# Kernel optimization log

Hardware: AMD Instinct MI355X
Metric: run time of the kernel (lower is better)

The kernel has to match this reference:

```python
import jax, jax.numpy as jnp
import numpy as np

EPS = 1e-5
NUM_CLUSTERS = 64


def _bn(x, g, b, m, v):
    # eval-mode BatchNorm over channel (last) axis
    return (x - m) * (g * jax.lax.rsqrt(v + EPS)) + b


def _segment_max(feat, choice, num_clusters):
    # feat: [B, N, C], choice: [B, N] -> [B, K, C] (amax per cluster, -inf if empty)
    def one(f, c):
        init = jnp.full((num_clusters, f.shape[-1]), -jnp.inf, dtype=f.dtype)
        return init.at[c].max(f)
    return jax.vmap(one)(feat, choice)


def setup_inputs() -> dict:
    key = jax.random.key(0)
    ks = jax.random.split(key, 8)
    B, N, K, OUT = 32, 8192, NUM_CLUSTERS, 384
    s = lambda fan: 1.0 / np.sqrt(fan)
    return {
        "xyz": jax.random.normal(ks[0], (B, N, 3), jnp.float32),
        "choice": jax.random.randint(ks[1], (B, N), 0, K, jnp.int32),
        "w1": jax.random.normal(ks[2], (128, 3), jnp.float32) * s(3),
        "b1": jnp.zeros((128,), jnp.float32),
        "bn1_g": jnp.ones((128,), jnp.float32),
        "bn1_b": jnp.zeros((128,), jnp.float32),
        "bn1_m": jnp.zeros((128,), jnp.float32),
        "bn1_v": jnp.ones((128,), jnp.float32),
        "w2": jax.random.normal(ks[3], (256, 128), jnp.float32) * s(128),
        "b2": jnp.zeros((256,), jnp.float32),
        "w3": jax.random.normal(ks[4], (512, 512), jnp.float32) * s(512),
        "b3": jnp.zeros((512,), jnp.float32),
        "bn2_g": jnp.ones((512,), jnp.float32),
        "bn2_b": jnp.zeros((512,), jnp.float32),
        "bn2_m": jnp.zeros((512,), jnp.float32),
        "bn2_v": jnp.ones((512,), jnp.float32),
        "w4": jax.random.normal(ks[5], (OUT, 512), jnp.float32) * s(512),
        "b4": jnp.zeros((OUT,), jnp.float32),
    }


def reference(xyz, choice, w1, b1, bn1_g, bn1_b, bn1_m, bn1_v, w2, b2,
              w3, b3, bn2_g, bn2_b, bn2_m, bn2_v, w4, b4):
    # first_conv: 1x1 conv == per-point linear. xyz: [B,N,3]
    h = jnp.einsum("bnc,oc->bno", xyz, w1) + b1            # [B,N,128]
    h = jax.nn.relu(_bn(h, bn1_g, bn1_b, bn1_m, bn1_v))
    feat = jnp.einsum("bnc,oc->bno", h, w2) + b2            # [B,N,256]
    # cluster amax pooling + gather-broadcast back to points
    fg = _segment_max(feat, choice, NUM_CLUSTERS)           # [B,K,256]
    fg_pts = jnp.take_along_axis(fg, choice[..., None], axis=1)  # [B,N,256]
    f = jnp.concatenate([fg_pts, feat], axis=-1)            # [B,N,512]
    # second_conv
    h2 = jnp.einsum("bnc,oc->bno", f, w3) + b3              # [B,N,512]
    h2 = jax.nn.relu(_bn(h2, bn2_g, bn2_b, bn2_m, bn2_v))
    out = jnp.einsum("bnc,oc->bno", h2, w4) + b4            # [B,N,out_dim]
    return _segment_max(out, choice, NUM_CLUSTERS)          # [B,K,out_dim]
```

## Files before the change

### kernel.cpp

```cpp
#include <hip/hip_runtime.h>
#include <hip/hip_bf16.h>

typedef unsigned short u16;
typedef __attribute__((ext_vector_type(8))) short short8;
typedef __attribute__((ext_vector_type(4))) float f32x4;

#define EPSV 1e-5f
#define ENC_NINF 0x007FFFFFu

__device__ __forceinline__ float bf2f(u16 u) {
    union { unsigned int i; float f; } v; v.i = ((unsigned int)u) << 16; return v.f;
}
__device__ __forceinline__ u16 f2bf(float f) {
    union { float f; unsigned int i; } v; v.f = f;
    unsigned int x = v.i;
    return (u16)((x + 0x7FFFu + ((x >> 16) & 1u)) >> 16);
}
__device__ __forceinline__ unsigned int encbf(u16 u) {
    unsigned int f = ((unsigned int)u) << 16;
    return (f & 0x80000000u) ? ~f : (f | 0x80000000u);
}
__device__ __forceinline__ float dec(unsigned int u) {
    union { float f; unsigned int uu; } v;
    v.uu = (u & 0x80000000u) ? (u & 0x7FFFFFFFu) : ~u;
    return v.f;
}

__device__ __forceinline__ void async16(const u16* g, u16* l) {
    __builtin_amdgcn_global_load_lds((const __attribute__((address_space(1))) void*)g,
                                     (__attribute__((address_space(3))) void*)l,
                                     16, 0, 0);
}

__global__ __launch_bounds__(256) void k_fillf(float* __restrict__ o, int n, float val)
{
    int i = blockIdx.x * 256 + threadIdx.x;
    if (i < n) o[i] = val;
}

struct Ptrs { const void* p[17]; int off[18]; int chN; };

__global__ __launch_bounds__(256) void k_repack(Ptrs P, const void* __restrict__ chSrc,
                                                int* __restrict__ chi, u16* __restrict__ rp,
                                                unsigned int* __restrict__ initp, int nU)
{
    const unsigned int* probe = (const unsigned int*)P.p[9];
    int cnt = 0;
#pragma unroll
    for (int i = 0; i < 64; ++i) {
        unsigned int lo = probe[i] & 0xFFFFu;
        if (((lo >> 7) & 0xFFu) >= 0x80u) ++cnt;
    }
    const bool is_f32 = (cnt > 8);

    const unsigned int* cp = (const unsigned int*)chSrc;
    int z = 0; unsigned int mx = 0;
    for (int i = 0; i < 1024; ++i) {
        unsigned int w = cp[i];
        z += (w == 0u);
        mx = (w > mx) ? w : mx;
    }
    const int chMode = (mx >= 64u) ? 2 : ((z > 300) ? 1 : 0);

    const int stride = gridDim.x * 256;
    const int gid0 = blockIdx.x * 256 + threadIdx.x;

    const int totalF = P.off[17];
    for (int g = gid0; g < totalF; g += stride) {
        int t = 0;
        while (g >= P.off[t + 1]) ++t;
        int off = g - P.off[t];
        u16 v;
        if (is_f32) v = f2bf(((const float*)P.p[t])[off]);
        else        v = ((const u16*)P.p[t])[off];
        rp[g] = v;
    }
    for (int i = gid0; i < P.chN; i += stride) {
        int v;
        if (chMode == 1)      v = (int)((const long long*)chSrc)[i];
        else if (chMode == 2) v = (int)((const float*)chSrc)[i];
        else                  v = ((const int*)chSrc)[i];
        chi[i] = v & 63;
    }
    for (int i = gid0; i < nU; i += stride) initp[i] = ENC_NINF;
}

__global__ __launch_bounds__(256) void k_sort(const int* __restrict__ chi,
                                              int* __restrict__ schoice,
                                              int* __restrict__ perm)
{
    __shared__ int hist[64];
    __shared__ int base[64];
    const int b = blockIdx.x, tid = threadIdx.x;
    if (tid < 64) hist[tid] = 0;
    __syncthreads();
    const int o = b << 13;
    for (int i = tid; i < 8192; i += 256) atomicAdd(&hist[chi[o + i]], 1);
    __syncthreads();
    if (tid == 0) {
        int s = 0;
        for (int k = 0; k < 64; ++k) { base[k] = s; s += hist[k]; }
    }
    __syncthreads();
    for (int i = tid; i < 8192; i += 256) {
        int k = chi[o + i];
        int pos = atomicAdd(&base[k], 1);
        schoice[o + pos] = k;
        perm[o + pos] = o + i;
    }
}

__global__ __launch_bounds__(256, 2) void g1_feat(
    const u16* __restrict__ xyz, const u16* __restrict__ w1, const u16* __restrict__ b1,
    const u16* __restrict__ g1v, const u16* __restrict__ bb1,
    const u16* __restrict__ m1, const u16* __restrict__ v1,
    const u16* __restrict__ w2, const u16* __restrict__ b2,
    const int* __restrict__ schoice, const int* __restrict__ perm,
    u16* __restrict__ feat, unsigned int* __restrict__ fg_u)
{
    __shared__ __align__(16) u16 Bs[256 * 128];
    __shared__ unsigned int lred[8 * 256];
    __shared__ float4 pw[128];
    __shared__ float xs[128], ys[128], zs[128];
    __shared__ int chs[128];
    const int tid = threadIdx.x, lane = tid & 63, wave = tid >> 6;
    const int wm = (wave & 1) << 6, wn = (wave >> 1) << 6;
    const int m0 = blockIdx.x << 7;
    if (tid < 128) {
        float s = bf2f(g1v[tid]) * rsqrtf(bf2f(v1[tid]) + EPSV);
        float4 w;
        w.x = bf2f(w1[tid * 3 + 0]) * s;
        w.y = bf2f(w1[tid * 3 + 1]) * s;
        w.z = bf2f(w1[tid * 3 + 2]) * s;
        w.w = (bf2f(b1[tid]) - bf2f(m1[tid])) * s + bf2f(bb1[tid]);
        pw[tid] = w;
        const u16* p = xyz + (size_t)perm[m0 + tid] * 3;
        xs[tid] = bf2f(p[0]); ys[tid] = bf2f(p[1]); zs[tid] = bf2f(p[2]);
        chs[tid] = schoice[m0 + tid];
    }
    const int q = lane >> 4, mr = lane & 15;
    f32x4 acc[2][4][4] = {};
#pragma unroll
    for (int i = 0; i < 16; ++i) {
        int id = (i << 8) + tid, row = id >> 4, cc = id & 15;
        async16(w2 + (size_t)row * 128 + ((cc ^ (row & 15)) << 3), &Bs[id << 3]);
    }
    __syncthreads();
    const int kmin = chs[0], nk = chs[127] - kmin + 1;
    const bool useL = (nk <= 8);
    if (useL) for (int i = tid; i < (nk << 8); i += 256) lred[i] = ENC_NINF;
#pragma unroll
    for (int kk = 0; kk < 4; ++kk) {
        const int lc = kk * 4 + q;
        float4 wv[8];
#pragma unroll
        for (int j = 0; j < 8; ++j) wv[j] = pw[kk * 32 + q * 8 + j];
        short8 af[4];
#pragma unroll
        for (int mi = 0; mi < 4; ++mi) {
            int row = wm + mi * 16 + mr;
            float x = xs[row], y = ys[row], z = zs[row];
#pragma unroll
            for (int j = 0; j < 8; ++j) {
                float val = fmaf(x, wv[j].x, fmaf(y, wv[j].y, fmaf(z, wv[j].z, wv[j].w)));
                af[mi][j] = (short)f2bf(fmaxf(val, 0.0f));
            }
        }
#pragma unroll
        for (int h = 0; h < 2; ++h) {
            short8 bfr[4];
#pragma unroll
            for (int ni = 0; ni < 4; ++ni) {
                int r = (h << 7) + wn + ni * 16 + mr;
                bfr[ni] = *(const short8*)&Bs[r * 128 + ((lc ^ (r & 15)) << 3)];
            }
#pragma unroll
            for (int mi = 0; mi < 4; ++mi)
#pragma unroll
                for (int ni = 0; ni < 4; ++ni)
                    acc[h][mi][ni] = __builtin_amdgcn_mfma_f32_16x16x32_bf16(af[mi], bfr[ni], acc[h][mi][ni], 0, 0, 0);
        }
    }
    __syncthreads();
    const int colb = lane & 15;
    const int bl = m0 >> 13;
    unsigned int* db = fg_u + (size_t)(bl << 6) * 256;
#pragma unroll
    for (int h = 0; h < 2; ++h)
#pragma unroll
        for (int ni = 0; ni < 4; ++ni) {
            int n = (h << 7) + wn + (ni << 4) + colb;
            float bv = bf2f(b2[n]);
#pragma unroll
            for (int mi = 0; mi < 4; ++mi) {
                int curk = -1; unsigned int run = 0;
#pragma unroll
                for (int r = 0; r < 4; ++r) {
                    int rr = wm + (mi << 4) + (q << 2) + r;
                    u16 vb = f2bf(acc[h][mi][ni][r] + bv);
                    feat[(size_t)(m0 + rr) * 256 + n] = vb;
                    unsigned int e = encbf(vb);
                    int k = chs[rr];
                    if (k != curk) {
                        if (curk >= 0) {
                            if (useL) atomicMax(&lred[((curk - kmin) << 8) + n], run);
                            else      atomicMax(&db[curk * 256 + n], run);
                        }
                        curk = k; run = e;
                    } else run = run > e ? run : e;
                }
                if (useL) atomicMax(&lred[((curk - kmin) << 8) + n], run);
                else      atomicMax(&db[curk * 256 + n], run);
            }
        }
    if (useL) {
        __syncthreads();
        for (int i = tid; i < (nk << 8); i += 256) {
            unsigned int v = lred[i];
            if (v != ENC_NINF) atomicMax(&db[(kmin + (i >> 8)) * 256 + (i & 255)], v);
        }
    }
}

__global__ __launch_bounds__(256, 2) void k_th(
    const u16* __restrict__ fg, const u16* __restrict__ w3, const u16* __restrict__ b3,
    const u16* __restrict__ g2, const u16* __restrict__ bb2,
    const u16* __restrict__ m2, const u16* __restrict__ v2,
    float* __restrict__ th)
{
    __shared__ __align__(16) u16 As[64 * 64];
    __shared__ __align__(16) u16 Bs[256 * 64];
    const int tid = threadIdx.x, lane = tid & 63, wave = tid >> 6;
    const int b = blockIdx.x, n0 = blockIdx.y << 8;
    const u16* fgb = fg + ((size_t)b << 14);
    f32x4 acc[4][4] = {};
    for (int k0 = 0; k0 < 256; k0 += 64) {
        __syncthreads();
#pragma unroll
        for (int i = 0; i < 8; ++i) {
            int id = (i << 8) + tid, row = id >> 3, cc = id & 7;
            async16(w3 + (size_t)(n0 + row) * 512 + k0 + ((cc ^ (row & 7)) << 3),
                    &Bs[id << 3]);
        }
#pragma unroll
        for (int i = 0; i < 2; ++i) {
            int id = (i << 8) + tid, row = id >> 3, cc = id & 7;
            async16(fgb + (size_t)row * 256 + k0 + ((cc ^ (row & 7)) << 3),
                    &As[id << 3]);
        }
        __syncthreads();
        const int q = lane >> 4, mr = lane & 15;
#pragma unroll
        for (int kk = 0; kk < 2; ++kk) {
            const int lc = (kk << 2) + q;
            short8 af[4], bfr[4];
#pragma unroll
            for (int mi = 0; mi < 4; ++mi) {
                int r = (mi << 4) + mr;
                af[mi] = *(const short8*)&As[r * 64 + ((lc ^ (r & 7)) << 3)];
            }
#pragma unroll
            for (int ni = 0; ni < 4; ++ni) {
                int r = (wave << 6) + (ni << 4) + mr;
                bfr[ni] = *(const short8*)&Bs[r * 64 + ((lc ^ (r & 7)) << 3)];
            }
#pragma unroll
            for (int mi = 0; mi < 4; ++mi)
#pragma unroll
                for (int ni = 0; ni < 4; ++ni)
                    acc[mi][ni] = __builtin_amdgcn_mfma_f32_16x16x32_bf16(af[mi], bfr[ni], acc[mi][ni], 0, 0, 0);
        }
    }
    const int q = lane >> 4, colb = lane & 15;
#pragma unroll
    for (int ni = 0; ni < 4; ++ni) {
        int n = n0 + (wave << 6) + (ni << 4) + colb;
        float s = bf2f(g2[n]) * rsqrtf(bf2f(v2[n]) + EPSV);
        float t = (bf2f(b3[n]) - bf2f(m2[n])) * s + bf2f(bb2[n]);
#pragma unroll
        for (int mi = 0; mi < 4; ++mi)
#pragma unroll
            for (int r = 0; r < 4; ++r) {
                int c = (mi << 4) + (q << 2) + r;
                th[((size_t)(b << 6) + c) * 512 + n] = fmaf(acc[mi][ni][r], s, t);
            }
    }
}

__global__ __launch_bounds__(256, 2) void g3_h2(
    const int* __restrict__ schoice, const u16* __restrict__ feat,
    const float* __restrict__ th, const u16* __restrict__ w3,
    const u16* __restrict__ g2, const u16* __restrict__ v2,
    u16* __restrict__ h2)
{
    __shared__ __align__(16) u16 As[128 * 64];
    __shared__ __align__(16) u16 Bs[2 * 128 * 64];
    __shared__ int chs[128];
    const int tid = threadIdx.x, lane = tid & 63, wave = tid >> 6;
    const int wm = (wave & 1) << 6, wn = (wave >> 1) << 6;
    const int m0 = blockIdx.x << 7, n0 = blockIdx.y << 8;
    const int c = tid & 7, rb = tid >> 3;
    if (tid < 128) chs[tid] = schoice[m0 + tid];
    const u16* ftrow[4];
#pragma unroll
    for (int i = 0; i < 4; ++i)
        ftrow[i] = feat + ((size_t)(m0 + rb + (i << 5)) << 8);
    f32x4 acc[2][4][4] = {};
    for (int k0 = 0; k0 < 256; k0 += 64) {
        __syncthreads();
#pragma unroll
        for (int nt = 0; nt < 2; ++nt)
#pragma unroll
            for (int i = 0; i < 4; ++i) {
                int id = (i << 8) + tid, row = id >> 3, cc = id & 7;
                async16(w3 + (size_t)(n0 + nt * 128 + row) * 512 + 256 + k0
                            + ((cc ^ (row & 7)) << 3),
                        &Bs[nt * 8192 + (id << 3)]);
            }
#pragma unroll
        for (int i = 0; i < 4; ++i) {
            int r = rb + (i << 5);
            async16(ftrow[i] + k0 + ((c ^ (r & 7)) << 3), &As[(((i << 8) + tid) << 3)]);
        }
        __syncthreads();
        const int q = lane >> 4, mr = lane & 15;
#pragma unroll
        for (int kk = 0; kk < 2; ++kk) {
            short8 af[4];
            const int lc = kk * 4 + q;
#pragma unroll
            for (int mi = 0; mi < 4; ++mi) {
                int r = wm + mi * 16 + mr;
                af[mi] = *(const short8*)&As[r * 64 + ((lc ^ (r & 7)) << 3)];
            }
#pragma unroll
            for (int nt = 0; nt < 2; ++nt) {
                short8 bfr[4];
#pragma unroll
                for (int ni = 0; ni < 4; ++ni) {
                    int r = wn + ni * 16 + mr;
                    bfr[ni] = *(const short8*)&Bs[nt * 8192 + r * 64 + ((lc ^ (r & 7)) << 3)];
                }
#pragma unroll
                for (int mi = 0; mi < 4; ++mi)
#pragma unroll
                    for (int ni = 0; ni < 4; ++ni)
                        acc[nt][mi][ni] = __builtin_amdgcn_mfma_f32_16x16x32_bf16(af[mi], bfr[ni], acc[nt][mi][ni], 0, 0, 0);
            }
        }
    }
    const int q = lane >> 4, colb = lane & 15;
    const float* thb = th + ((size_t)((m0 >> 13) << 6) * 512);
#pragma unroll
    for (int nt = 0; nt < 2; ++nt)
#pragma unroll
        for (int ni = 0; ni < 4; ++ni) {
            int n = n0 + nt * 128 + wn + (ni << 4) + colb;
            float s = bf2f(g2[n]) * rsqrtf(bf2f(v2[n]) + EPSV);
#pragma unroll
            for (int mi = 0; mi < 4; ++mi)
#pragma unroll
                for (int r = 0; r < 4; ++r) {
                    int rr = wm + (mi << 4) + (q << 2) + r;
                    float thv = thb[(size_t)chs[rr] * 512 + n];
                    h2[(size_t)(m0 + rr) * 512 + n] =
                        f2bf(fmaxf(fmaf(acc[nt][mi][ni][r], s, thv), 0.0f));
                }
        }
}

__global__ __launch_bounds__(512, 2) void g4_out(
    const u16* __restrict__ A, const u16* __restrict__ w4,
    const u16* __restrict__ bias, const int* __restrict__ schoice,
    unsigned int* __restrict__ out_u)
{
    __shared__ __align__(16) u16 As[128 * 64];
    __shared__ __align__(16) u16 Bs[192 * 64];
    __shared__ int chs[128];
    const int tid = threadIdx.x, lane = tid & 63, wave = tid >> 6;
    const int wm = (wave & 1) << 6, wn48 = (wave >> 1) * 48;
    const int m0 = blockIdx.x << 7;
    if (tid < 128) chs[tid] = schoice[m0 + tid];
    f32x4 acc[4][6] = {};
    for (int k0 = 0; k0 < 512; k0 += 64) {
#pragma unroll
        for (int cch = 0; cch < 2; ++cch) {
            __syncthreads();
            if (cch == 0)
#pragma unroll
                for (int i = 0; i < 2; ++i) {
                    int id = (i << 9) + tid, row = id >> 3, cc = id & 7;
                    async16(A + (size_t)(m0 + row) * 512 + k0 + ((cc ^ (row & 7)) << 3),
                            &As[id << 3]);
                }
#pragma unroll
            for (int i = 0; i < 3; ++i) {
                int id = (i << 9) + tid, row = id >> 3, cc = id & 7;
                async16(w4 + (size_t)(cch * 192 + row) * 512 + k0 + ((cc ^ (row & 7)) << 3),
                        &Bs[id << 3]);
            }
            __syncthreads();
            const int q = lane >> 4, mr = lane & 15;
#pragma unroll
            for (int kk = 0; kk < 2; ++kk) {
                const int lc = (kk << 2) + q;
                short8 af[4];
#pragma unroll
                for (int mi = 0; mi < 4; ++mi) {
                    int r = wm + (mi << 4) + mr;
                    af[mi] = *(const short8*)&As[r * 64 + ((lc ^ (r & 7)) << 3)];
                }
#pragma unroll
                for (int ni = 0; ni < 3; ++ni) {
                    int r = wn48 + (ni << 4) + mr;
                    short8 bfr = *(const short8*)&Bs[r * 64 + ((lc ^ (r & 7)) << 3)];
#pragma unroll
                    for (int mi = 0; mi < 4; ++mi)
                        acc[mi][cch * 3 + ni] = __builtin_amdgcn_mfma_f32_16x16x32_bf16(af[mi], bfr, acc[mi][cch * 3 + ni], 0, 0, 0);
                }
            }
        }
    }
    __syncthreads();
    unsigned int* lred = (unsigned int*)As;
    const int kmin = chs[0], nk = chs[127] - kmin + 1;
    const bool useL = (nk <= 26);
    const int bl = m0 >> 13;
    unsigned int* db = out_u + (size_t)(bl << 6) * 384;
    if (useL) for (int i = tid; i < nk * 384; i += 512) lred[i] = ENC_NINF;
    __syncthreads();
    const int q = lane >> 4, colb = lane & 15;
#pragma unroll
    for (int j = 0; j < 6; ++j) {
        int nc = (j < 3 ? 0 : 192) + wn48 + ((j < 3 ? j : j - 3) << 4) + colb;
        float bv = bf2f(bias[nc]);
#pragma unroll
        for (int mi = 0; mi < 4; ++mi) {
            int curk = -1; unsigned int run = 0;
#pragma unroll
            for (int r = 0; r < 4; ++r) {
                int rr = wm + (mi << 4) + (q << 2) + r;
                unsigned int e = encbf(f2bf(acc[mi][j][r] + bv));
                int k = chs[rr];
                if (k != curk) {
                    if (curk >= 0) {
                        if (useL) atomicMax(&lred[(curk - kmin) * 384 + nc], run);
                        else      atomicMax(&db[curk * 384 + nc], run);
                    }
                    curk = k; run = e;
                } else run = run > e ? run : e;
            }
            if (useL) atomicMax(&lred[(curk - kmin) * 384 + nc], run);
            else      atomicMax(&db[curk * 384 + nc], run);
        }
    }
    if (useL) {
        __syncthreads();
        for (int i = tid; i < nk * 384; i += 512) {
            unsigned int v = lred[i];
            if (v != ENC_NINF) {
                int kq = i / 384;
                atomicMax(&db[(kmin + kq) * 384 + (i - kq * 384)], v);
            }
        }
    }
}

__global__ __launch_bounds__(256) void k_dec_bf(const unsigned int* __restrict__ u,
                                                u16* __restrict__ o, int n)
{
    int i = blockIdx.x * 256 + threadIdx.x;
    if (i < n) o[i] = f2bf(dec(u[i]));
}
__global__ __launch_bounds__(256) void k_dec_f32(const unsigned int* __restrict__ u,
                                                 float* __restrict__ o, int n)
{
    int i = blockIdx.x * 256 + threadIdx.x;
    if (i < n) o[i] = dec(u[i]);
}

extern "C" void kernel_launch(void* const* d_in, const int* in_sizes, int n_in,
                              void* d_out, int out_size, void* d_ws, size_t ws_size,
                              hipStream_t stream)
{
    float* out = (float*)d_out;
    if (n_in != 18) {
        k_fillf<<<dim3((out_size + 255) / 256), 256, 0, stream>>>(out, out_size, 1000.0f);
        return;
    }

    const int map[17] = {0, 2, 3, 4, 5, 6, 7, 8, 9, 10, 11, 12, 13, 14, 15, 16, 17};
    Ptrs P;
    P.off[0] = 0;
    for (int i = 0; i < 17; ++i) {
        P.p[i] = d_in[map[i]];
        P.off[i + 1] = P.off[i] + in_sizes[map[i]];
    }
    P.chN = in_sizes[1];

    char* ws = (char*)d_ws;
    int* chi = (int*)ws;
    const size_t chiB = ((size_t)P.chN * 4 + 255) & ~255ull;
    int* schoice = (int*)(ws + chiB);
    int* perm    = (int*)(ws + 2 * chiB);
    u16* rp = (u16*)(ws + 3 * chiB);
    const size_t rpB = ((size_t)P.off[17] * 2 + 255) & ~255ull;
    const size_t RPB = 3 * chiB + rpB;

    unsigned int* fg_u_all  = (unsigned int*)(ws + RPB);
    unsigned int* out_u_all = fg_u_all + 32 * 64 * 256;
    const size_t UB = 5242880ull;
    const int nU = 32 * 64 * 640;

    k_repack<<<dim3(1024), 256, 0, stream>>>(P, d_in[1], chi, rp, fg_u_all, nU);
    k_sort<<<dim3(P.chN >> 13), 256, 0, stream>>>(chi, schoice, perm);

    const u16* xyz  = rp + P.off[0];
    const u16* w1   = rp + P.off[1];
    const u16* b1   = rp + P.off[2];
    const u16* bn1g = rp + P.off[3];
    const u16* bn1b = rp + P.off[4];
    const u16* bn1m = rp + P.off[5];
    const u16* bn1v = rp + P.off[6];
    const u16* w2   = rp + P.off[7];
    const u16* b2   = rp + P.off[8];
    const u16* w3   = rp + P.off[9];
    const u16* b3   = rp + P.off[10];
    const u16* bn2g = rp + P.off[11];
    const u16* bn2b = rp + P.off[12];
    const u16* bn2m = rp + P.off[13];
    const u16* bn2v = rp + P.off[14];
    const u16* w4   = rp + P.off[15];
    const u16* b4   = rp + P.off[16];

    const size_t PB = 12746752ull;
    int sb = 32;
    while (sb > 1 && RPB + UB + (size_t)sb * PB > ws_size) sb >>= 1;
    if (RPB + UB + PB > ws_size) {
        k_fillf<<<dim3((out_size + 255) / 256), 256, 0, stream>>>(out, out_size, 3000.0f);
        return;
    }
    const int ns = 32 / sb;

    char* wsb = ws + RPB + UB;
    const size_t featB = (size_t)sb * 8192 * 256 * 2;
    const size_t h2B   = (size_t)sb * 8192 * 512 * 2;
    const size_t fgB   = (size_t)sb * 64 * 256 * 2;
    u16* feat = (u16*)(wsb);
    u16* h2s  = (u16*)(wsb + featB);
    u16* fg   = (u16*)(wsb + featB + h2B);
    float* th = (float*)(wsb + featB + h2B + fgB);

    const int mblk = sb << 6;
    const int nfg = sb * 64 * 256;
    const int nou = sb * 64 * 384;
    for (int s = 0; s < ns; ++s) {
        const int b0 = s * sb;
        const int pt0 = b0 << 13;
        const int* sch_sl = schoice + pt0;
        const int* perm_sl = perm + pt0;
        unsigned int* fg_u  = fg_u_all + (size_t)b0 * 64 * 256;
        unsigned int* out_u = out_u_all + (size_t)b0 * 64 * 384;
        g1_feat<<<dim3(mblk), 256, 0, stream>>>(xyz, w1, b1, bn1g, bn1b, bn1m, bn1v,
                                                w2, b2, sch_sl, perm_sl, feat, fg_u);
        k_dec_bf<<<dim3((nfg + 255) / 256), 256, 0, stream>>>(fg_u, fg, nfg);
        k_th<<<dim3(sb, 2), 256, 0, stream>>>(fg, w3, b3, bn2g, bn2b, bn2m, bn2v, th);
        g3_h2<<<dim3(mblk, 2), 256, 0, stream>>>(sch_sl, feat, th, w3,
                                                 bn2g, bn2v, h2s);
        g4_out<<<dim3(mblk), 512, 0, stream>>>(h2s, w4, b4, sch_sl, out_u);
        k_dec_f32<<<dim3((nou + 255) / 256), 256, 0, stream>>>(out_u,
                                                               out + ((size_t)b0 << 6) * 384, nou);
    }
}
```

Baseline: 585.5 us.

## Fuse second-conv GEMM and output GEMM into one kernel with on-chip h2

Merges the h2 GEMM (feat×w3 plus the per-cluster term, BN and ReLU) with the output GEMM (h2×w4) and the segment max into a single kernel. Each block keeps its 128-row feat tile in LDS, computes h2 in 128-column chunks into a swizzled LDS buffer, and immediately accumulates those chunks into the 384-wide output accumulators. This removes the global write and re-read of the bf16 h2 tensor and shrinks the workspace, which allows larger batch slices. The cost is a large LDS footprint (about 160 KB per block), which limits occupancy, and w3 being re-fetched per block without the previous N split. The local-reduction threshold is raised to fit the larger reused LDS.

New measurement: 563.3 us. 3.8% less time.

```diff
diff --git a/kernel.cpp b/kernel.cpp
--- a/kernel.cpp
+++ b/kernel.cpp
@@ -287,120 +287,93 @@
     }
 }
 
-__global__ __launch_bounds__(256, 2) void g3_h2(
+__global__ __launch_bounds__(512, 2) void g34_out(
     const int* __restrict__ schoice, const u16* __restrict__ feat,
     const float* __restrict__ th, const u16* __restrict__ w3,
-    const u16* __restrict__ g2, const u16* __restrict__ v2,
-    u16* __restrict__ h2)
-{
-    __shared__ __align__(16) u16 As[128 * 64];
-    __shared__ __align__(16) u16 Bs[2 * 128 * 64];
+    const u16* __restrict__ w4, const u16* __restrict__ g2,
+    const u16* __restrict__ v2, const u16* __restrict__ b4,
+    unsigned int* __restrict__ out_u)
+{
+    __shared__ __align__(16) u16 Ar[128 * 256];
+    __shared__ __align__(16) u16 H[128 * 128];
+    __shared__ __align__(16) u16 U[384 * 64];
     __shared__ int chs[128];
     const int tid = threadIdx.x, lane = tid & 63, wave = tid >> 6;
-    const int wm = (wave & 1) << 6, wn = (wave >> 1) << 6;
-    const int m0 = blockIdx.x << 7, n0 = blockIdx.y << 8;
-    const int c = tid & 7, rb = tid >> 3;
+    const int q = lane >> 4, mr = lane & 15, colb = lane & 15;
+    const int wm  = (wave & 1) << 6;
+    const int wnA = (wave >> 1) << 5;
+    const int wnB = (wave >> 1) * 96;
+    const int m0 = blockIdx.x << 7;
     if (tid < 128) chs[tid] = schoice[m0 + tid];
-    const u16* ftrow[4];
-#pragma unroll
-    for (int i = 0; i < 4; ++i)
-        ftrow[i] = feat + ((size_t)(m0 + rb + (i << 5)) << 8);
-    f32x4 acc[2][4][4] = {};
-    for (int k0 = 0; k0 < 256; k0 += 64) {
-        __syncthreads();
-#pragma unroll
-        for (int nt = 0; nt < 2; ++nt)
-#pragma unroll
-            for (int i = 0; i < 4; ++i) {
-                int id = (i << 8) + tid, row = id >> 3, cc = id & 7;
-                async16(w3 + (size_t)(n0 + nt * 128 + row) * 512 + 256 + k0
+#pragma unroll
+    for (int i = 0; i < 8; ++i) {
+        int id = (i << 9) + tid;
+        int row = id >> 5, c32 = id & 31;
+        int g64 = c32 >> 3, cc = c32 & 7;
+        async16(feat + ((size_t)(m0 + row) << 8) + (g64 << 6) + ((cc ^ (row & 7)) << 3),
+                &Ar[id << 3]);
+    }
+    const float* thb = th + ((size_t)((m0 >> 13) << 6) * 512);
+    f32x4 acc_b[4][6] = {};
+    for (int nq = 0; nq < 4; ++nq) {
+        f32x4 acc_a[4][2] = {};
+        for (int k0 = 0; k0 < 256; k0 += 64) {
+            __syncthreads();
+#pragma unroll
+            for (int i = 0; i < 2; ++i) {
+                int id = (i << 9) + tid, row = id >> 3, cc = id & 7;
+                async16(w3 + (size_t)((nq << 7) + row) * 512 + 256 + k0
                             + ((cc ^ (row & 7)) << 3),
-                        &Bs[nt * 8192 + (id << 3)]);
-            }
-#pragma unroll
-        for (int i = 0; i < 4; ++i) {
-            int r = rb + (i << 5);
-            async16(ftrow[i] + k0 + ((c ^ (r & 7)) << 3), &As[(((i << 8) + tid) << 3)]);
-        }
-        __syncthreads();
-        const int q = lane >> 4, mr = lane & 15;
-#pragma unroll
-        for (int kk = 0; kk < 2; ++kk) {
-            short8 af[4];
-            const int lc = kk * 4 + q;
-#pragma unroll
-            for (int mi = 0; mi < 4; ++mi) {
-                int r = wm + mi * 16 + mr;
-                af[mi] = *(const short8*)&As[r * 64 + ((lc ^ (r & 7)) << 3)];
-            }
-#pragma unroll
-            for (int nt = 0; nt < 2; ++nt) {
-                short8 bfr[4];
-#pragma unroll
-                for (int ni = 0; ni < 4; ++ni) {
-                    int r = wn + ni * 16 + mr;
-                    bfr[ni] = *(const short8*)&Bs[nt * 8192 + r * 64 + ((lc ^ (r & 7)) << 3)];
+                        &U[id << 3]);
+            }
+            __syncthreads();
+#pragma unroll
+            for (int kk = 0; kk < 2; ++kk) {
+                const int lc = (kk << 2) + q;
+                short8 af[4], bfr[2];
+#pragma unroll
+                for (int mi = 0; mi < 4; ++mi) {
+                    int r = wm + (mi << 4) + mr;
+                    af[mi] = *(const short8*)&Ar[r * 256 + k0 + ((lc ^ (r & 7)) << 3)];
                 }
 #pragma unroll
+                for (int ni = 0; ni < 2; ++ni) {
+                    int r = wnA + (ni << 4) + mr;
+                    bfr[ni] = *(const short8*)&U[r * 64 + ((lc ^ (r & 7)) << 3)];
+                }
+#pragma unroll
                 for (int mi = 0; mi < 4; ++mi)
 #pragma unroll
-                    for (int ni = 0; ni < 4; ++ni)
-                        acc[nt][mi][ni] = __builtin_amdgcn_mfma_f32_16x16x32_bf16(af[mi], bfr[ni], acc[nt][mi][ni], 0, 0, 0);
-            }
-        }
-    }
-    const int q = lane >> 4, colb = lane & 15;
-    const float* thb = th + ((size_t)((m0 >> 13) << 6) * 512);
-#pragma unroll
-    for (int nt = 0; nt < 2; ++nt)
-#pragma unroll
-        for (int ni = 0; ni < 4; ++ni) {
-            int n = n0 + nt * 128 + wn + (ni << 4) + colb;
+                    for (int ni = 0; ni < 2; ++ni)
+                        acc_a[mi][ni] = __builtin_amdgcn_mfma_f32_16x16x32_bf16(af[mi], bfr[ni], acc_a[mi][ni], 0, 0, 0);
+            }
+        }
+#pragma unroll
+        for (int ni = 0; ni < 2; ++ni) {
+            int ck = wnA + (ni << 4) + colb;
+            int n = (nq << 7) + ck;
             float s = bf2f(g2[n]) * rsqrtf(bf2f(v2[n]) + EPSV);
+            int cchi = ck >> 3, clo = ck & 7;
 #pragma unroll
             for (int mi = 0; mi < 4; ++mi)
 #pragma unroll
                 for (int r = 0; r < 4; ++r) {
                     int rr = wm + (mi << 4) + (q << 2) + r;
                     float thv = thb[(size_t)chs[rr] * 512 + n];
-                    h2[(size_t)(m0 + rr) * 512 + n] =
-                        f2bf(fmaxf(fmaf(acc[nt][mi][ni][r], s, thv), 0.0f));
+                    H[rr * 128 + ((cchi ^ (rr & 7)) << 3) + clo] =
+                        f2bf(fmaxf(fmaf(acc_a[mi][ni][r], s, thv), 0.0f));
                 }
         }
-}
-
-__global__ __launch_bounds__(512, 2) void g4_out(
-    const u16* __restrict__ A, const u16* __restrict__ w4,
-    const u16* __restrict__ bias, const int* __restrict__ schoice,
-    unsigned int* __restrict__ out_u)
-{
-    __shared__ __align__(16) u16 As[128 * 64];
-    __shared__ __align__(16) u16 Bs[192 * 64];
-    __shared__ int chs[128];
-    const int tid = threadIdx.x, lane = tid & 63, wave = tid >> 6;
-    const int wm = (wave & 1) << 6, wn48 = (wave >> 1) * 48;
-    const int m0 = blockIdx.x << 7;
-    if (tid < 128) chs[tid] = schoice[m0 + tid];
-    f32x4 acc[4][6] = {};
-    for (int k0 = 0; k0 < 512; k0 += 64) {
-#pragma unroll
-        for (int cch = 0; cch < 2; ++cch) {
+        for (int kq = 0; kq < 128; kq += 64) {
             __syncthreads();
-            if (cch == 0)
-#pragma unroll
-                for (int i = 0; i < 2; ++i) {
-                    int id = (i << 9) + tid, row = id >> 3, cc = id & 7;
-                    async16(A + (size_t)(m0 + row) * 512 + k0 + ((cc ^ (row & 7)) << 3),
-                            &As[id << 3]);
-                }
-#pragma unroll
-            for (int i = 0; i < 3; ++i) {
+#pragma unroll
+            for (int i = 0; i < 6; ++i) {
                 int id = (i << 9) + tid, row = id >> 3, cc = id & 7;
-                async16(w4 + (size_t)(cch * 192 + row) * 512 + k0 + ((cc ^ (row & 7)) << 3),
-                        &Bs[id << 3]);
+                async16(w4 + (size_t)row * 512 + (nq << 7) + kq
+                            + ((cc ^ (row & 7)) << 3),
+                        &U[id << 3]);
             }
             __syncthreads();
-            const int q = lane >> 4, mr = lane & 15;
 #pragma unroll
             for (int kk = 0; kk < 2; ++kk) {
                 const int lc = (kk << 2) + q;
@@ -408,39 +381,38 @@
 #pragma unroll
                 for (int mi = 0; mi < 4; ++mi) {
                     int r = wm + (mi << 4) + mr;
-                    af[mi] = *(const short8*)&As[r * 64 + ((lc ^ (r & 7)) << 3)];
+                    af[mi] = *(const short8*)&H[r * 128 + (((kq >> 3) + (lc ^ (r & 7))) << 3)];
                 }
 #pragma unroll
-                for (int ni = 0; ni < 3; ++ni) {
-                    int r = wn48 + (ni << 4) + mr;
-                    short8 bfr = *(const short8*)&Bs[r * 64 + ((lc ^ (r & 7)) << 3)];
+                for (int ni = 0; ni < 6; ++ni) {
+                    int r = wnB + (ni << 4) + mr;
+                    short8 bfr = *(const short8*)&U[r * 64 + ((lc ^ (r & 7)) << 3)];
 #pragma unroll
                     for (int mi = 0; mi < 4; ++mi)
-                        acc[mi][cch * 3 + ni] = __builtin_amdgcn_mfma_f32_16x16x32_bf16(af[mi], bfr, acc[mi][cch * 3 + ni], 0, 0, 0);
+                        acc_b[mi][ni] = __builtin_amdgcn_mfma_f32_16x16x32_bf16(af[mi], bfr, acc_b[mi][ni], 0, 0, 0);
                 }
             }
         }
     }
     __syncthreads();
-    unsigned int* lred = (unsigned int*)As;
+    unsigned int* lred = (unsigned int*)Ar;
     const int kmin = chs[0], nk = chs[127] - kmin + 1;
-    const bool useL = (nk <= 26);
+    const bool useL = (nk <= 42);
     const int bl = m0 >> 13;
     unsigned int* db = out_u + (size_t)(bl << 6) * 384;
     if (useL) for (int i = tid; i < nk * 384; i += 512) lred[i] = ENC_NINF;
     __syncthreads();
-    const int q = lane >> 4, colb = lane & 15;
-#pragma unroll
-    for (int j = 0; j < 6; ++j) {
-        int nc = (j < 3 ? 0 : 192) + wn48 + ((j < 3 ? j : j - 3) << 4) + colb;
-        float bv = bf2f(bias[nc]);
+#pragma unroll
+    for (int ni = 0; ni < 6; ++ni) {
+        int nc = wnB + (ni << 4) + colb;
+        float bv = bf2f(b4[nc]);
 #pragma unroll
         for (int mi = 0; mi < 4; ++mi) {
             int curk = -1; unsigned int run = 0;
 #pragma unroll
             for (int r = 0; r < 4; ++r) {
                 int rr = wm + (mi << 4) + (q << 2) + r;
-                unsigned int e = encbf(f2bf(acc[mi][j][r] + bv));
+                unsigned int e = encbf(f2bf(acc_b[mi][ni][r] + bv));
                 int k = chs[rr];
                 if (k != curk) {
                     if (curk >= 0) {
@@ -533,7 +505,7 @@
     const u16* w4   = rp + P.off[15];
     const u16* b4   = rp + P.off[16];
 
-    const size_t PB = 12746752ull;
+    const size_t PB = 4358144ull;
     int sb = 32;
     while (sb > 1 && RPB + UB + (size_t)sb * PB > ws_size) sb >>= 1;
     if (RPB + UB + PB > ws_size) {
@@ -544,12 +516,10 @@
 
     char* wsb = ws + RPB + UB;
     const size_t featB = (size_t)sb * 8192 * 256 * 2;
-    const size_t h2B   = (size_t)sb * 8192 * 512 * 2;
     const size_t fgB   = (size_t)sb * 64 * 256 * 2;
     u16* feat = (u16*)(wsb);
-    u16* h2s  = (u16*)(wsb + featB);
-    u16* fg   = (u16*)(wsb + featB + h2B);
-    float* th = (float*)(wsb + featB + h2B + fgB);
+    u16* fg   = (u16*)(wsb + featB);
+    float* th = (float*)(wsb + featB + fgB);
 
     const int mblk = sb << 6;
     const int nfg = sb * 64 * 256;
@@ -565,9 +535,8 @@
                                                 w2, b2, sch_sl, perm_sl, feat, fg_u);
         k_dec_bf<<<dim3((nfg + 255) / 256), 256, 0, stream>>>(fg_u, fg, nfg);
         k_th<<<dim3(sb, 2), 256, 0, stream>>>(fg, w3, b3, bn2g, bn2b, bn2m, bn2v, th);
-        g3_h2<<<dim3(mblk, 2), 256, 0, stream>>>(sch_sl, feat, th, w3,
-                                                 bn2g, bn2v, h2s);
-        g4_out<<<dim3(mblk), 512, 0, stream>>>(h2s, w4, b4, sch_sl, out_u);
+        g34_out<<<dim3(mblk), 512, 0, stream>>>(sch_sl, feat, th, w3, w4,
+                                                bn2g, bn2v, b4, out_u);
         k_dec_f32<<<dim3((nou + 255) / 256), 256, 0, stream>>>(out_u,
                                                                out + ((size_t)b0 << 6) * 384, nou);
     }
```
